# Performance work log

Hardware: AMD Instinct MI355X
Metric: run time of the kernel (lower is better)

Reference implementation:

```python
import jax, jax.numpy as jnp
import numpy as np

EPS = 1e-5
P, B, T, C = 2, 8, 1024, 1024
H = 4 * C

def layernorm(x, g, b):
    mu = jnp.mean(x, axis=-1, keepdims=True)
    var = jnp.var(x, axis=-1, keepdims=True)
    return (x - mu) * jax.lax.rsqrt(var + EPS) * g + b

def time_shift(x):
    # ZeroPad2d((0,0,1,-1)): xx[t] = x[t-1], xx[0] = 0 along the T axis
    pad = [(0, 0)] * (x.ndim - 2) + [(1, 0), (0, 0)]
    return jnp.pad(x, pad)[..., :-1, :]

def wkv(time_decay, time_first, k, v):
    # Faithful port of the RWKV-v4 CUDA WKV scan (numerically stable form).
    # k, v: [N, T, C]; time_decay/time_first: [C]
    w = -jnp.exp(time_decay)  # decay (negative)
    u = time_first
    kT = jnp.moveaxis(k, 1, 0)  # [T, N, C]
    vT = jnp.moveaxis(v, 1, 0)
    N = k.shape[0]
    Cc = k.shape[2]

    def step(carry, kv):
        aa, bb, pp = carry
        kk, vv = kv
        ww = u + kk
        p = jnp.maximum(pp, ww)
        e1 = jnp.exp(pp - p)
        e2 = jnp.exp(ww - p)
        y = (e1 * aa + e2 * vv) / (e1 * bb + e2)
        ww2 = w + pp
        p2 = jnp.maximum(ww2, kk)
        e1b = jnp.exp(ww2 - p2)
        e2b = jnp.exp(kk - p2)
        return (e1b * aa + e2b * vv, e1b * bb + e2b, p2), y

    init = (jnp.zeros((N, Cc), jnp.float32), jnp.zeros((N, Cc), jnp.float32),
            jnp.full((N, Cc), -1e38, jnp.float32))
    _, yT = jax.lax.scan(step, init, (kT, vT))
    return jnp.moveaxis(yT, 0, 1)  # [N, T, C]


def setup_inputs() -> dict:
    key = jax.random.key(0)
    ks = jax.random.split(key, 20)
    f32 = jnp.float32
    layer_id, n_layer = 1, 12
    ratio_0_to_1 = layer_id / (n_layer - 1)
    ratio_1_to_almost0 = 1.0 - layer_id / n_layer
    xcurve = (np.arange(C, dtype=np.float32) / C).reshape(1, 1, C)
    decay_speed = -5 + 8 * (np.arange(C, dtype=np.float32) / (C - 1)) ** (0.7 + 1.3 * ratio_0_to_1)
    zigzag = (np.array([(i + 1) % 3 - 1 for i in range(C)], dtype=np.float32)) * 0.5
    time_first = np.ones(C, dtype=np.float32) * np.log(0.3) + zigzag
    mk = np.stack([xcurve ** ratio_1_to_almost0 for _ in range(P)], 0)  # [P,1,1,C]
    mv = np.stack([xcurve ** ratio_1_to_almost0 + 0.3 * ratio_0_to_1 for _ in range(P)], 0)
    mr = np.stack([xcurve ** (0.5 * ratio_1_to_almost0) for _ in range(P)], 0)
    s = 0.02
    return {
        'x': jax.random.normal(ks[0], (P, B, T, C), f32),
        'ln1_g': jnp.ones((C,), f32), 'ln1_b': jnp.zeros((C,), f32),
        'ln2_g': jnp.ones((C,), f32), 'ln2_b': jnp.zeros((C,), f32),
        'time_decay': jnp.asarray(decay_speed, f32),
        'time_first': jnp.asarray(time_first, f32),
        'att_mix_k': jnp.asarray(mk, f32), 'att_mix_v': jnp.asarray(mv, f32),
        'att_mix_r': jnp.asarray(mr, f32),
        'Wk': jax.random.normal(ks[1], (C, C), f32) * s,
        'Wv': jax.random.normal(ks[2], (C, C), f32) * s,
        'Wr': jax.random.normal(ks[3], (C, C), f32) * s,
        'Wo': jax.random.normal(ks[4], (C, C), f32) * s,
        'cm_mix_k': jnp.asarray(mk, f32), 'cm_mix_r': jnp.asarray(mk, f32),
        'Wck': jax.random.normal(ks[5], (H, C), f32) * s,
        'Wcr': jax.random.normal(ks[6], (C, C), f32) * s,
        'Wcv': jax.random.normal(ks[7], (C, H), f32) * s,
    }


def reference(x, ln1_g, ln1_b, ln2_g, ln2_b, time_decay, time_first,
              att_mix_k, att_mix_v, att_mix_r, Wk, Wv, Wr, Wo,
              cm_mix_k, cm_mix_r, Wck, Wcr, Wcv):
    p, b, t, c = x.shape
    # --- TimeMix branch: x = x + Wo @ (sigmoid(r) * WKV(k, v)) ---
    h = layernorm(x, ln1_g, ln1_b)
    xx = time_shift(h)
    xk = h * att_mix_k + xx * (1 - att_mix_k)
    xv = h * att_mix_v + xx * (1 - att_mix_v)
    xr = h * att_mix_r + xx * (1 - att_mix_r)
    k = jnp.einsum('pbtc,dc->pbtd', xk, Wk)
    v = jnp.einsum('pbtc,dc->pbtd', xv, Wv)
    sr = jax.nn.sigmoid(jnp.einsum('pbtc,dc->pbtd', xr, Wr))
    y = wkv(time_decay, time_first,
            k.reshape(p * b, t, c), v.reshape(p * b, t, c)).reshape(p, b, t, c)
    x = x + jnp.einsum('pbtc,dc->pbtd', sr * y, Wo)
    # --- ChannelMix branch ---
    h = layernorm(x, ln2_g, ln2_b)
    xx = time_shift(h)
    xk = h * cm_mix_k + xx * (1 - cm_mix_k)
    xr = h * cm_mix_r + xx * (1 - cm_mix_r)
    kk = jnp.einsum('pbtc,hc->pbth', xk, Wck)
    kk = jnp.square(jax.nn.relu(kk))
    kv = jnp.einsum('pbth,ch->pbtc', kk, Wcv)
    out = jax.nn.sigmoid(jnp.einsum('pbtc,dc->pbtd', xr, Wcr)) * kv
    return x + out
```

## Files before the change

kernel.cpp:

```cpp
#include <hip/hip_runtime.h>

#define T_SEQ 1024
#define C_DIM 1024
#define H_DIM 4096
#define M_ROWS 16384
#define CHUNKS 16
#define CLEN 64

typedef _Float16 f16x8 __attribute__((ext_vector_type(8)));
typedef _Float16 f16x4 __attribute__((ext_vector_type(4)));
typedef float    f32x4 __attribute__((ext_vector_type(4)));

#define AS1 __attribute__((address_space(1)))
#define AS3 __attribute__((address_space(3)))

__device__ __forceinline__ void gload_lds16(const void* g, void* l) {
  __builtin_amdgcn_global_load_lds((const AS1 void*)g, (AS3 void*)l, 16, 0, 0);
}

__device__ __forceinline__ float sigmoidf_(float x) {
  return 1.0f / (1.0f + __expf(-x));
}

struct CvtArgs {
  const float* src[7];
  _Float16*    dst[7];
  int n4[7];
  int start[8];
};

__global__ __launch_bounds__(256) void cvt_all_kernel(CvtArgs a) {
  const int bid = blockIdx.x;
  int s = 0;
#pragma unroll
  for (int j = 0; j < 7; ++j) s += (bid >= a.start[j + 1]) ? 1 : 0;
  const int i = (bid - a.start[s]) * 256 + threadIdx.x;
  if (i >= a.n4[s]) return;
  f32x4 v = reinterpret_cast<const f32x4*>(a.src[s])[i];
  f16x4 o;
  o[0] = (_Float16)v[0]; o[1] = (_Float16)v[1];
  o[2] = (_Float16)v[2]; o[3] = (_Float16)v[3];
  reinterpret_cast<f16x4*>(a.dst[s])[i] = o;
}

template<int NMIX>
__global__ __launch_bounds__(512) void lnmix_kernel(const float* __restrict__ x,
    const float* __restrict__ g, const float* __restrict__ b,
    const float* __restrict__ mk, const float* __restrict__ mv,
    const float* __restrict__ mr,
    _Float16* __restrict__ xk, _Float16* __restrict__ xv,
    _Float16* __restrict__ xr) {
  const int wave = threadIdx.x >> 6;
  const int lane = threadIdx.x & 63;
  const int row  = blockIdx.x * 8 + wave;
  const int t    = row & (T_SEQ - 1);
  const int p    = row >> 13;
  const f32x4* x0 = reinterpret_cast<const f32x4*>(x + (size_t)row * C_DIM);
  const f32x4* x1 = reinterpret_cast<const f32x4*>(x + (size_t)(row - 1) * C_DIM);
  f32x4 vc[4], vp[4];
  float s0 = 0.f, q0 = 0.f, s1 = 0.f, q1 = 0.f;
#pragma unroll
  for (int i = 0; i < 4; ++i) {
    vc[i] = x0[i * 64 + lane];
#pragma unroll
    for (int j = 0; j < 4; ++j) { s0 += vc[i][j]; q0 += vc[i][j] * vc[i][j]; }
    if (t) {
      vp[i] = x1[i * 64 + lane];
#pragma unroll
      for (int j = 0; j < 4; ++j) { s1 += vp[i][j]; q1 += vp[i][j] * vp[i][j]; }
    }
  }
#pragma unroll
  for (int off = 32; off > 0; off >>= 1) {
    s0 += __shfl_xor(s0, off, 64);
    q0 += __shfl_xor(q0, off, 64);
    s1 += __shfl_xor(s1, off, 64);
    q1 += __shfl_xor(q1, off, 64);
  }
  const float mu0   = s0 * (1.0f / C_DIM);
  const float rstd0 = rsqrtf(q0 * (1.0f / C_DIM) - mu0 * mu0 + 1e-5f);
  const float mu1   = s1 * (1.0f / C_DIM);
  const float rstd1 = rsqrtf(q1 * (1.0f / C_DIM) - mu1 * mu1 + 1e-5f);
  const f32x4* g4  = reinterpret_cast<const f32x4*>(g);
  const f32x4* b4  = reinterpret_cast<const f32x4*>(b);
  const f32x4* mk4 = reinterpret_cast<const f32x4*>(mk + (size_t)p * C_DIM);
  const f32x4* mv4 = NMIX == 3 ? reinterpret_cast<const f32x4*>(mv + (size_t)p * C_DIM) : nullptr;
  const f32x4* mr4 = reinterpret_cast<const f32x4*>(mr + (size_t)p * C_DIM);
  f16x4* xk4 = reinterpret_cast<f16x4*>(xk) + (size_t)row * 256;
  f16x4* xv4 = NMIX == 3 ? reinterpret_cast<f16x4*>(xv) + (size_t)row * 256 : nullptr;
  f16x4* xr4 = reinterpret_cast<f16x4*>(xr) + (size_t)row * 256;
#pragma unroll
  for (int i = 0; i < 4; ++i) {
    const f32x4 gg = g4[i * 64 + lane];
    const f32x4 bb = b4[i * 64 + lane];
    const f32x4 ak = mk4[i * 64 + lane];
    const f32x4 ar = mr4[i * 64 + lane];
    f32x4 av;
    if (NMIX == 3) av = mv4[i * 64 + lane];
    f16x4 ok, ov, orr;
#pragma unroll
    for (int j = 0; j < 4; ++j) {
      const float hc = (vc[i][j] - mu0) * rstd0 * gg[j] + bb[j];
      const float hp = t ? ((vp[i][j] - mu1) * rstd1 * gg[j] + bb[j]) : 0.f;
      ok[j] = (_Float16)(hc * ak[j] + hp * (1.f - ak[j]));
      orr[j] = (_Float16)(hc * ar[j] + hp * (1.f - ar[j]));
      if (NMIX == 3) ov[j] = (_Float16)(hc * av[j] + hp * (1.f - av[j]));
    }
    xk4[i * 64 + lane] = ok;
    xr4[i * 64 + lane] = orr;
    if (NMIX == 3) xv4[i * 64 + lane] = ov;
  }
}

__global__ __launch_bounds__(1024, 1) void wkv_kernel(const _Float16* __restrict__ k,
    const _Float16* __restrict__ v, const _Float16* __restrict__ r,
    const float* __restrict__ td, const float* __restrict__ tf,
    _Float16* __restrict__ a_out) {
  __shared__ float sA[CHUNKS][64];
  __shared__ float sB[CHUNKS][64];
  __shared__ float sP[CHUNKS][64];
  const int tid   = threadIdx.x;
  const int chunk = tid >> 6;
  const int ch    = tid & 63;
  const int n     = blockIdx.x >> 4;
  const int cg    = blockIdx.x & 15;
  const int c     = cg * 64 + ch;
  const float w = -__expf(td[c]);
  const float u = tf[c];
  const size_t cbase = (size_t)n * T_SEQ * C_DIM + (size_t)chunk * CLEN * C_DIM + c;

  float aa = 0.f, bb = 0.f, pp = -1e38f;
  for (int s = 0; s < CLEN; ++s) {
    const size_t idx = cbase + (size_t)s * C_DIM;
    const float kk = (float)k[idx];
    const float vv = (float)v[idx];
    const float ww2 = w + pp;
    const float p2  = fmaxf(ww2, kk);
    const float e1b = __expf(ww2 - p2);
    const float e2b = __expf(kk - p2);
    aa = e1b * aa + e2b * vv;
    bb = e1b * bb + e2b;
    pp = p2;
  }
  sA[chunk][ch] = aa; sB[chunk][ch] = bb; sP[chunk][ch] = pp;
  __syncthreads();

  if (chunk == 0) {
    float pa = 0.f, pb = 0.f, ppr = -1e38f;
    const float wL = w * (float)CLEN;
    for (int j = 0; j < CHUNKS; ++j) {
      const float la = sA[j][ch], lb = sB[j][ch], lp = sP[j][ch];
      sA[j][ch] = pa; sB[j][ch] = pb; sP[j][ch] = ppr;
      const float dp = wL + ppr;
      const float np = fmaxf(dp, lp);
      const float e1 = __expf(dp - np);
      const float e2 = __expf(lp - np);
      pa  = e1 * pa + e2 * la;
      pb  = e1 * pb + e2 * lb;
      ppr = np;
    }
  }
  __syncthreads();

  aa = sA[chunk][ch]; bb = sB[chunk][ch]; pp = sP[chunk][ch];
  for (int s = 0; s < CLEN; ++s) {
    const size_t idx = cbase + (size_t)s * C_DIM;
    const float kk = (float)k[idx];
    const float vv = (float)v[idx];
    const float ww = u + kk;
    const float p  = fmaxf(pp, ww);
    const float e1 = __expf(pp - p);
    const float e2 = __expf(ww - p);
    const float yv = __fdividef(e1 * aa + e2 * vv, e1 * bb + e2);
    const float sr = sigmoidf_((float)r[idx]);
    a_out[idx] = (_Float16)(sr * yv);
    const float ww2 = w + pp;
    const float p2  = fmaxf(ww2, kk);
    const float e1b = __expf(ww2 - p2);
    const float e2b = __expf(kk - p2);
    aa = e1b * aa + e2b * vv;
    bb = e1b * bb + e2b;
    pp = p2;
  }
}

#define GBAR() do { __builtin_amdgcn_sched_barrier(0); \
                    __builtin_amdgcn_s_barrier(); \
                    __builtin_amdgcn_sched_barrier(0); } while (0)
#define WVN(n) do { asm volatile("s_waitcnt vmcnt(" #n ")" ::: "memory"); \
                    __builtin_amdgcn_sched_barrier(0); } while (0)
#define WLN(n) do { asm volatile("s_waitcnt lgkmcnt(" #n ")" ::: "memory"); \
                    __builtin_amdgcn_sched_barrier(0); } while (0)
#define SCHED() __builtin_amdgcn_sched_barrier(0)
#define STAGE(op, SRC, row0, k0, bb) do { \
    _Pragma("unroll") \
    for (int c_ = 0; c_ < 2; ++c_) { \
      gload_lds16((SRC) + (size_t)((row0) + c_ * 64) * K + (k0), \
                  &lds[bb][op][((size_t)((row0) + c_ * 64) << 6) + dbase]); \
    } } while (0)
#define RD_AH(dst, mh) do { \
    _Pragma("unroll") for (int i_ = 0; i_ < 4; ++i_) \
    _Pragma("unroll") for (int k_ = 0; k_ < 2; ++k_) \
      dst[i_][k_] = *reinterpret_cast<const f16x8*>( \
        &lds[bi][0][((wr * 128 + (mh) * 64 + i_ * 16 + frow) << 6) + \
                    (((k_ << 5) + fk) ^ fxorh)]); \
  } while (0)
#define RD_BH(dst, nh) do { \
    _Pragma("unroll") for (int j_ = 0; j_ < 2; ++j_) \
    _Pragma("unroll") for (int k_ = 0; k_ < 2; ++k_) \
      dst[j_][k_] = *reinterpret_cast<const f16x8*>( \
        &lds[bi][1][((wcn * 64 + (nh) * 32 + j_ * 16 + frow) << 6) + \
                    (((k_ << 5) + fk) ^ fxorh)]); \
  } while (0)
#define MM16(asrc, bsrc, mh, nh) do { \
    _Pragma("unroll") for (int k_ = 0; k_ < 2; ++k_) \
    _Pragma("unroll") for (int i_ = 0; i_ < 4; ++i_) \
    _Pragma("unroll") for (int j_ = 0; j_ < 2; ++j_) \
      acc[(mh) * 4 + i_][(nh) * 2 + j_] = __builtin_amdgcn_mfma_f32_16x16x32_f16( \
        asrc[i_][k_], bsrc[j_][k_], acc[(mh) * 4 + i_][(nh) * 2 + j_], 0, 0, 0); \
  } while (0)

template<int EPI>
__global__ __launch_bounds__(512, 2) void gemm_nt_256(
    const _Float16* __restrict__ A, const _Float16* __restrict__ B,
    void* __restrict__ Cv, const float* __restrict__ X,
    const _Float16* __restrict__ KV, int M, int N, int K,
    size_t strideA, size_t strideB, size_t strideCbytes) {
  __shared__ _Float16 lds[2][2][256 * 64];
  const int tid  = threadIdx.x;
  const int wave = tid >> 6;
  const int lane = tid & 63;
  const int wr   = wave >> 2;
  const int wcn  = wave & 3;

  A  = A + (size_t)blockIdx.z * strideA;
  B  = B + (size_t)blockIdx.z * strideB;
  Cv = (void*)((char*)Cv + (size_t)blockIdx.z * strideCbytes);

  const unsigned nwx  = gridDim.x;
  const unsigned pery = gridDim.y >> 3;
  const unsigned id   = blockIdx.y * nwx + blockIdx.x;
  const unsigned xcd  = id & 7;
  const unsigned loc  = id >> 3;
  const size_t m0 = (size_t)(xcd * pery + loc / nwx) * 256;
  const size_t n0 = (size_t)(loc % nwx) * 256;

  const int srow  = tid >> 3;
  const int scolh = ((tid & 7) ^ (srow & 7)) << 3;
  const size_t dbase = (size_t)(srow & ~7) << 6;
  const _Float16* sA = A + (m0 + srow) * (size_t)K + scolh;
  const _Float16* sB = B + (n0 + srow) * (size_t)K + scolh;

  const int frow  = lane & 15;
  const int fk    = (lane >> 4) << 3;
  const int fxorh = (frow & 7) << 3;

  f32x4 acc[8][4];
#pragma unroll
  for (int i = 0; i < 8; ++i)
#pragma unroll
    for (int j = 0; j < 4; ++j) acc[i][j] = (f32x4){0.f, 0.f, 0.f, 0.f};

  const int NT = K >> 6;
  STAGE(0, sA, 0,   0, 0);
  STAGE(1, sB, 0,   0, 0);
  STAGE(1, sB, 128, 0, 0);
  STAGE(0, sA, 128, 0, 0);
  if (NT > 1) {
    STAGE(0, sA, 0, 64, 1);
    STAGE(1, sB, 0, 64, 1);
    WVN(4);
  } else {
    WVN(0);
  }
  GBAR();

  for (int t = 0; t < NT; ++t) {
    const int bi = t & 1;
    const int nb = bi ^ 1;
    const int k1 = (t + 1) << 6;
    const int k2 = (t + 2) << 6;
    const bool s1 = (t + 1) < NT;
    const bool s2 = (t + 2) < NT;
    f16x8 a0[4][2], a1[4][2], b0[2][2], b1[2][2];
    RD_AH(a0, 0); RD_BH(b0, 0); SCHED();
    if (s1) STAGE(1, sB, 128, k1, nb);
    WLN(8);
    GBAR();
    WLN(0);
    MM16(a0, b0, 0, 0);
    GBAR();
    RD_BH(b1, 1); SCHED();
    if (s1) STAGE(0, sA, 128, k1, nb);
    GBAR();
    WLN(0);
    MM16(a0, b1, 0, 1);
    GBAR();
    RD_AH(a1, 1); SCHED();
    if (s2) STAGE(0, sA, 0, k2, bi);
    GBAR();
    WLN(0);
    MM16(a1, b0, 1, 0);
    GBAR();
    if (s2) {
      STAGE(1, sB, 0, k2, bi);
      WVN(4);
    } else {
      WVN(0);
    }
    GBAR();
    WLN(0);
    MM16(a1, b1, 1, 1);
    GBAR();
  }

  const int ecol  = lane & 15;
  const int erow4 = (lane >> 4) * 4;
#pragma unroll
  for (int mf = 0; mf < 8; ++mf)
#pragma unroll
    for (int nf = 0; nf < 4; ++nf) {
      const size_t rbase = m0 + (size_t)(wr * 128 + mf * 16 + erow4);
      const size_t cc    = n0 + (size_t)(wcn * 64 + nf * 16 + ecol);
#pragma unroll
      for (int r = 0; r < 4; ++r) {
        const float val = acc[mf][nf][r];
        const size_t off = (rbase + r) * (size_t)N + cc;
        if constexpr (EPI == 0) {
          ((_Float16*)Cv)[off] = (_Float16)val;
        } else if constexpr (EPI == 1) {
          const float tq = fmaxf(val, 0.f);
          ((_Float16*)Cv)[off] = (_Float16)(tq * tq);
        } else if constexpr (EPI == 2) {
          ((float*)Cv)[off] = val + X[off];
        } else {
          ((float*)Cv)[off] = X[off] + sigmoidf_(val) * (float)KV[off];
        }
      }
    }
}

extern "C" void kernel_launch(void* const* d_in, const int* in_sizes, int n_in,
                              void* d_out, int out_size, void* d_ws, size_t ws_size,
                              hipStream_t stream) {
  const float* x      = (const float*)d_in[0];
  const float* ln1_g  = (const float*)d_in[1];
  const float* ln1_b  = (const float*)d_in[2];
  const float* ln2_g  = (const float*)d_in[3];
  const float* ln2_b  = (const float*)d_in[4];
  const float* tdec   = (const float*)d_in[5];
  const float* tfirst = (const float*)d_in[6];
  const float* amk    = (const float*)d_in[7];
  const float* amv    = (const float*)d_in[8];
  const float* amr    = (const float*)d_in[9];
  const float* Wk     = (const float*)d_in[10];
  const float* Wv     = (const float*)d_in[11];
  const float* Wr     = (const float*)d_in[12];
  const float* Wo     = (const float*)d_in[13];
  const float* cmk    = (const float*)d_in[14];
  const float* cmr    = (const float*)d_in[15];
  const float* Wck    = (const float*)d_in[16];
  const float* Wcr    = (const float*)d_in[17];
  const float* Wcv    = (const float*)d_in[18];

  char* ws = (char*)d_ws;
  const size_t SZ = (size_t)M_ROWS * C_DIM * sizeof(_Float16);
  _Float16* B0 = (_Float16*)(ws + 0 * SZ);
  _Float16* B1 = (_Float16*)(ws + 1 * SZ);
  _Float16* B2 = (_Float16*)(ws + 2 * SZ);
  _Float16* B3 = (_Float16*)(ws + 3 * SZ);
  _Float16* B4 = (_Float16*)(ws + 4 * SZ);
  _Float16* B5 = (_Float16*)(ws + 5 * SZ);
  _Float16* B6 = (_Float16*)(ws + 6 * SZ);
  _Float16* wWk  = (_Float16*)(ws + 7 * SZ);
  _Float16* wWv  = wWk  + (size_t)C_DIM * C_DIM;
  _Float16* wWr  = wWv  + (size_t)C_DIM * C_DIM;
  _Float16* wWo  = wWr  + (size_t)C_DIM * C_DIM;
  _Float16* wWcr = wWo  + (size_t)C_DIM * C_DIM;
  _Float16* wWck = wWcr + (size_t)C_DIM * C_DIM;
  _Float16* wWcv = wWck + (size_t)H_DIM * C_DIM;

  {
    CvtArgs a;
    const float* srcs[7] = {Wk, Wv, Wr, Wo, Wcr, Wck, Wcv};
    _Float16*    dsts[7] = {wWk, wWv, wWr, wWo, wWcr, wWck, wWcv};
    const size_t ns[7]   = {(size_t)C_DIM * C_DIM, (size_t)C_DIM * C_DIM,
                            (size_t)C_DIM * C_DIM, (size_t)C_DIM * C_DIM,
                            (size_t)C_DIM * C_DIM, (size_t)H_DIM * C_DIM,
                            (size_t)C_DIM * H_DIM};
    int st = 0;
    for (int j = 0; j < 7; ++j) {
      a.src[j] = srcs[j]; a.dst[j] = dsts[j];
      a.n4[j] = (int)(ns[j] / 4);
      a.start[j] = st;
      st += (a.n4[j] + 255) / 256;
    }
    a.start[7] = st;
    cvt_all_kernel<<<dim3(st), dim3(256), 0, stream>>>(a);
  }

  const dim3 gblk(512);
  const dim3 gLN(M_ROWS / 8);
  const dim3 gN1(C_DIM / 256, M_ROWS / 256);
  const dim3 gKVR(C_DIM / 256, M_ROWS / 256, 3);
  const dim3 gN4(H_DIM / 256, M_ROWS / 256);

  lnmix_kernel<3><<<gLN, gblk, 0, stream>>>(x, ln1_g, ln1_b, amk, amv, amr,
                                            B1, B2, B3);
  gemm_nt_256<0><<<gKVR, gblk, 0, stream>>>(B1, wWk, B4, nullptr, nullptr,
      M_ROWS, C_DIM, C_DIM,
      (size_t)M_ROWS * C_DIM, (size_t)C_DIM * C_DIM,
      (size_t)M_ROWS * C_DIM * sizeof(_Float16));
  wkv_kernel<<<dim3(256), dim3(1024), 0, stream>>>(B4, B5, B6, tdec, tfirst, B1);
  gemm_nt_256<2><<<gN1, gblk, 0, stream>>>(B1, wWo, d_out, x, nullptr,
      M_ROWS, C_DIM, C_DIM, 0, 0, 0);

  lnmix_kernel<2><<<gLN, gblk, 0, stream>>>((const float*)d_out, ln2_g, ln2_b,
                                            cmk, nullptr, cmr, B1, nullptr, B2);
  gemm_nt_256<1><<<gN4, gblk, 0, stream>>>(B1, wWck, B3, nullptr, nullptr,
      M_ROWS, H_DIM, C_DIM, 0, 0, 0);
  gemm_nt_256<0><<<gN1, gblk, 0, stream>>>(B3, wWcv, B1, nullptr, nullptr,
      M_ROWS, C_DIM, H_DIM, 0, 0, 0);
  gemm_nt_256<3><<<gN1, gblk, 0, stream>>>(B2, wWcr, d_out, (const float*)d_out, B1,
      M_ROWS, C_DIM, C_DIM, 0, 0, 0);
}
```

Baseline: 622.3 us.

## Use 4-wave 256x256 GEMM blocks with 128x128 per-wave tiles and simpler double buffering

The GEMM moves from 8 waves of 512 threads (each owning a 128x64 sub-tile) to 4 waves of 256 threads, each owning a 128x128 sub-tile with 64 accumulator fragments. This raises MFMA work per LDS read. The fine-grained four-phase interleaved pipeline is replaced by a plain double buffer: the full next K-tile is prefetched and one barrier is taken per iteration. The cost is much higher register pressure (256 accumulator VGPRs plus 32 operand vectors), one block per CU, and less overlap between global loads and compute. The layernorm kernels keep their 512-thread launch.

Measured after the change: 804.1 us. 29.2% more time.

```diff
diff --git a/kernel.cpp b/kernel.cpp
--- a/kernel.cpp
+++ b/kernel.cpp
@@ -192,46 +192,42 @@
 #define WLN(n) do { asm volatile("s_waitcnt lgkmcnt(" #n ")" ::: "memory"); \
                     __builtin_amdgcn_sched_barrier(0); } while (0)
 #define SCHED() __builtin_amdgcn_sched_barrier(0)
-#define STAGE(op, SRC, row0, k0, bb) do { \
+#define STAGEOP(op, SRCP, k0, bb) do { \
     _Pragma("unroll") \
-    for (int c_ = 0; c_ < 2; ++c_) { \
-      gload_lds16((SRC) + (size_t)((row0) + c_ * 64) * K + (k0), \
-                  &lds[bb][op][((size_t)((row0) + c_ * 64) << 6) + dbase]); \
+    for (int s_ = 0; s_ < 8; ++s_) { \
+      gload_lds16((SRCP) + (size_t)(s_ * 32) * K + (k0), \
+                  &lds[bb][op][((size_t)(s_ * 32) << 6) + dbase]); \
     } } while (0)
-#define RD_AH(dst, mh) do { \
-    _Pragma("unroll") for (int i_ = 0; i_ < 4; ++i_) \
-    _Pragma("unroll") for (int k_ = 0; k_ < 2; ++k_) \
-      dst[i_][k_] = *reinterpret_cast<const f16x8*>( \
-        &lds[bi][0][((wr * 128 + (mh) * 64 + i_ * 16 + frow) << 6) + \
-                    (((k_ << 5) + fk) ^ fxorh)]); \
+#define RD_A8(dst, ks) do { \
+    _Pragma("unroll") for (int i_ = 0; i_ < 8; ++i_) \
+      dst[i_] = *reinterpret_cast<const f16x8*>( \
+        &lds[bi][0][((size_t)(wr * 128 + i_ * 16 + frow) << 6) + \
+                    ((((ks) << 5) + fk) ^ fxorh)]); \
   } while (0)
-#define RD_BH(dst, nh) do { \
-    _Pragma("unroll") for (int j_ = 0; j_ < 2; ++j_) \
-    _Pragma("unroll") for (int k_ = 0; k_ < 2; ++k_) \
-      dst[j_][k_] = *reinterpret_cast<const f16x8*>( \
-        &lds[bi][1][((wcn * 64 + (nh) * 32 + j_ * 16 + frow) << 6) + \
-                    (((k_ << 5) + fk) ^ fxorh)]); \
+#define RD_B8(dst, ks) do { \
+    _Pragma("unroll") for (int j_ = 0; j_ < 8; ++j_) \
+      dst[j_] = *reinterpret_cast<const f16x8*>( \
+        &lds[bi][1][((size_t)(wc * 128 + j_ * 16 + frow) << 6) + \
+                    ((((ks) << 5) + fk) ^ fxorh)]); \
   } while (0)
-#define MM16(asrc, bsrc, mh, nh) do { \
-    _Pragma("unroll") for (int k_ = 0; k_ < 2; ++k_) \
-    _Pragma("unroll") for (int i_ = 0; i_ < 4; ++i_) \
-    _Pragma("unroll") for (int j_ = 0; j_ < 2; ++j_) \
-      acc[(mh) * 4 + i_][(nh) * 2 + j_] = __builtin_amdgcn_mfma_f32_16x16x32_f16( \
-        asrc[i_][k_], bsrc[j_][k_], acc[(mh) * 4 + i_][(nh) * 2 + j_], 0, 0, 0); \
+#define MM64(asrc, bsrc) do { \
+    _Pragma("unroll") for (int i_ = 0; i_ < 8; ++i_) \
+    _Pragma("unroll") for (int j_ = 0; j_ < 8; ++j_) \
+      acc[i_][j_] = __builtin_amdgcn_mfma_f32_16x16x32_f16( \
+        asrc[i_], bsrc[j_], acc[i_][j_], 0, 0, 0); \
   } while (0)
 
 template<int EPI>
-__global__ __launch_bounds__(512, 2) void gemm_nt_256(
+__global__ __launch_bounds__(256, 1) void gemm_nt_256(
     const _Float16* __restrict__ A, const _Float16* __restrict__ B,
     void* __restrict__ Cv, const float* __restrict__ X,
     const _Float16* __restrict__ KV, int M, int N, int K,
     size_t strideA, size_t strideB, size_t strideCbytes) {
   __shared__ _Float16 lds[2][2][256 * 64];
   const int tid  = threadIdx.x;
-  const int wave = tid >> 6;
   const int lane = tid & 63;
-  const int wr   = wave >> 2;
-  const int wcn  = wave & 3;
+  const int wr   = (tid >> 6) >> 1;
+  const int wc   = (tid >> 6) & 1;
 
   A  = A + (size_t)blockIdx.z * strideA;
   B  = B + (size_t)blockIdx.z * strideB;
@@ -255,62 +251,35 @@
   const int fk    = (lane >> 4) << 3;
   const int fxorh = (frow & 7) << 3;
 
-  f32x4 acc[8][4];
+  f32x4 acc[8][8];
 #pragma unroll
   for (int i = 0; i < 8; ++i)
 #pragma unroll
-    for (int j = 0; j < 4; ++j) acc[i][j] = (f32x4){0.f, 0.f, 0.f, 0.f};
+    for (int j = 0; j < 8; ++j) acc[i][j] = (f32x4){0.f, 0.f, 0.f, 0.f};
 
   const int NT = K >> 6;
-  STAGE(0, sA, 0,   0, 0);
-  STAGE(1, sB, 0,   0, 0);
-  STAGE(1, sB, 128, 0, 0);
-  STAGE(0, sA, 128, 0, 0);
-  if (NT > 1) {
-    STAGE(0, sA, 0, 64, 1);
-    STAGE(1, sB, 0, 64, 1);
-    WVN(4);
-  } else {
-    WVN(0);
-  }
-  GBAR();
+  STAGEOP(0, sA, 0, 0);
+  STAGEOP(1, sB, 0, 0);
 
   for (int t = 0; t < NT; ++t) {
     const int bi = t & 1;
     const int nb = bi ^ 1;
     const int k1 = (t + 1) << 6;
-    const int k2 = (t + 2) << 6;
-    const bool s1 = (t + 1) < NT;
-    const bool s2 = (t + 2) < NT;
-    f16x8 a0[4][2], a1[4][2], b0[2][2], b1[2][2];
-    RD_AH(a0, 0); RD_BH(b0, 0); SCHED();
-    if (s1) STAGE(1, sB, 128, k1, nb);
-    WLN(8);
-    GBAR();
-    WLN(0);
-    MM16(a0, b0, 0, 0);
-    GBAR();
-    RD_BH(b1, 1); SCHED();
-    if (s1) STAGE(0, sA, 128, k1, nb);
-    GBAR();
-    WLN(0);
-    MM16(a0, b1, 0, 1);
-    GBAR();
-    RD_AH(a1, 1); SCHED();
-    if (s2) STAGE(0, sA, 0, k2, bi);
-    GBAR();
-    WLN(0);
-    MM16(a1, b0, 1, 0);
-    GBAR();
-    if (s2) {
-      STAGE(1, sB, 0, k2, bi);
-      WVN(4);
+    if (t + 1 < NT) {
+      STAGEOP(0, sA, k1, nb);
+      STAGEOP(1, sB, k1, nb);
+      WVN(16);
     } else {
       WVN(0);
     }
     GBAR();
+    f16x8 a0[8], b0v[8], a1[8], b1v[8];
+    RD_A8(a0, 0); RD_B8(b0v, 0); SCHED();
+    RD_A8(a1, 1); RD_B8(b1v, 1); SCHED();
+    WLN(15);
+    MM64(a0, b0v);
     WLN(0);
-    MM16(a1, b1, 1, 1);
+    MM64(a1, b1v);
     GBAR();
   }
 
@@ -319,9 +288,9 @@
 #pragma unroll
   for (int mf = 0; mf < 8; ++mf)
 #pragma unroll
-    for (int nf = 0; nf < 4; ++nf) {
+    for (int nf = 0; nf < 8; ++nf) {
       const size_t rbase = m0 + (size_t)(wr * 128 + mf * 16 + erow4);
-      const size_t cc    = n0 + (size_t)(wcn * 64 + nf * 16 + ecol);
+      const size_t cc    = n0 + (size_t)(wc * 128 + nf * 16 + ecol);
 #pragma unroll
       for (int r = 0; r < 4; ++r) {
         const float val = acc[mf][nf][r];
@@ -399,14 +368,14 @@
     cvt_all_kernel<<<dim3(st), dim3(256), 0, stream>>>(a);
   }
 
-  const dim3 gblk(512);
+  const dim3 gblk(256);
   const dim3 gLN(M_ROWS / 8);
   const dim3 gN1(C_DIM / 256, M_ROWS / 256);
   const dim3 gKVR(C_DIM / 256, M_ROWS / 256, 3);
   const dim3 gN4(H_DIM / 256, M_ROWS / 256);
 
-  lnmix_kernel<3><<<gLN, gblk, 0, stream>>>(x, ln1_g, ln1_b, amk, amv, amr,
-                                            B1, B2, B3);
+  lnmix_kernel<3><<<gLN, dim3(512), 0, stream>>>(x, ln1_g, ln1_b, amk, amv, amr,
+                                                 B1, B2, B3);
   gemm_nt_256<0><<<gKVR, gblk, 0, stream>>>(B1, wWk, B4, nullptr, nullptr,
       M_ROWS, C_DIM, C_DIM,
       (size_t)M_ROWS * C_DIM, (size_t)C_DIM * C_DIM,
@@ -415,8 +384,8 @@
   gemm_nt_256<2><<<gN1, gblk, 0, stream>>>(B1, wWo, d_out, x, nullptr,
       M_ROWS, C_DIM, C_DIM, 0, 0, 0);
 
-  lnmix_kernel<2><<<gLN, gblk, 0, stream>>>((const float*)d_out, ln2_g, ln2_b,
-                                            cmk, nullptr, cmr, B1, nullptr, B2);
+  lnmix_kernel<2><<<gLN, dim3(512), 0, stream>>>((const float*)d_out, ln2_g, ln2_b,
+                                                 cmk, nullptr, cmr, B1, nullptr, B2);
   gemm_nt_256<1><<<gN4, gblk, 0, stream>>>(B1, wWck, B3, nullptr, nullptr,
       M_ROWS, H_DIM, C_DIM, 0, 0, 0);
   gemm_nt_256<0><<<gN1, gblk, 0, stream>>>(B3, wWcv, B1, nullptr, nullptr,
```
